# Performance work log

Hardware: AMD Instinct MI355X
Metric: run time of the kernel (lower is better)

The kernel has to match this reference:

```python
import jax, jax.numpy as jnp
import numpy as np

FRAME_LENGTH = 800
FRAME_STEP = 200
FFT_LENGTH = 800


def _hann_window(n):
    # tf.signal.hann_window default: periodic=True -> 0.5 - 0.5*cos(2*pi*k/n)
    k = jnp.arange(n, dtype=jnp.float32)
    return 0.5 - 0.5 * jnp.cos(2.0 * np.pi * k / n)


def setup_inputs() -> dict:
    key = jax.random.key(0)
    signals = jax.random.normal(key, (16, 240000), dtype=jnp.float32)
    window = _hann_window(FRAME_LENGTH)  # fft_length == frame_length, no pad
    n = jnp.arange(FFT_LENGTH, dtype=jnp.float32)
    angles = -2.0 * np.pi * n[:, None] * n[None, :] / float(FFT_LENGTH)  # [k, n]
    dft_cos = jnp.cos(angles)
    dft_sin = jnp.sin(angles)
    return {"signals": signals, "window": window, "dft_cos": dft_cos, "dft_sin": dft_sin}


def reference(signals, window, dft_cos, dft_sin):
    # Frame the signal: [B, num_frames, frame_length] via gather (pad_end=False)
    signal_length = signals.shape[1]
    num_frames = (signal_length - FRAME_LENGTH) // FRAME_STEP + 1
    starts = jnp.arange(num_frames, dtype=jnp.int32) * FRAME_STEP
    offsets = jnp.arange(FRAME_LENGTH, dtype=jnp.int32)
    idx = starts[:, None] + offsets[None, :]          # [F, L]
    frames = signals[:, idx]                          # [B, F, L]
    windowed = frames * window[:FRAME_LENGTH]         # [B, F, L]
    # Dense real/imag DFT: out[b,f,k] = sum_n windowed[b,f,n] * dft[k,n]
    real = jnp.einsum('bfn,kn->bfk', windowed, dft_cos)
    imag = jnp.einsum('bfn,kn->bfk', windowed, dft_sin)
    bins = FFT_LENGTH // 2 + 1
    return jnp.stack([real[:, :, :bins], imag[:, :, :bins]], axis=-1)  # [B, F, bins, 2]
```

## Files before the change

kernel.cpp:

```cpp
#include <hip/hip_runtime.h>
#include <hip/hip_bf16.h>

#define NBATCH   16
#define SIGLEN   240000
#define FRAMES   1197
#define M_TOTAL  (NBATCH * FRAMES)
#define K_TOTAL  800
#define NBINS    401
#define NOUT     (2 * NBINS)
#define FSTEP    200

#define KPAD  832
#define NTK   26
#define GBN   64
#define GNT   13
#define BSTR  840
#define NRG   1197
#define SCSTR 68

#define TMB   512
#define TMT   38
#define TNWG  (GNT * TMT)

#define GMB   1024
#define GMT   19
#define GNWG  (GNT * GMT)

#define SIG_ELEMS  ((size_t)NBATCH * SIGLEN)
#define B_WS_ELEMS ((size_t)(GNT * GBN) * KPAD)
#define APK_ELEMS  ((size_t)NRG * NTK * 64 * 8)
#define WS_TIER1   ((APK_ELEMS + B_WS_ELEMS) * 2)
#define WS_TIER2   ((SIG_ELEMS + B_WS_ELEMS) * 2)

#define PREP_B_BLOCKS 338
#define PREP_SIG_BLOCKS 1875
#define PACK_TOTAL (NRG * NTK * 64)
#define PACK_BLOCKS ((PACK_TOTAL + 255) / 256)

typedef float  f32x4  __attribute__((ext_vector_type(4)));
typedef __bf16 bf16x8 __attribute__((ext_vector_type(8)));

static __device__ __forceinline__ unsigned f2bf_pair(float lo, float hi) {
    union { float f; unsigned u; } a, b;
    a.f = lo; b.f = hi;
    unsigned ua = (a.u + 0x7fffu + ((a.u >> 16) & 1u)) >> 16;
    unsigned ub = (b.u + 0x7fffu + ((b.u >> 16) & 1u)) >> 16;
    return ua | (ub << 16);
}

__global__ __launch_bounds__(256) void prep_b(
    const float* __restrict__ dcos, const float* __restrict__ dsin,
    const float* __restrict__ wnd, ushort* __restrict__ B)
{
    int idx = blockIdx.x * 256 + threadIdx.x;
    int j  = idx / 104;
    int c8 = (idx - j * 104) * 8;
    uint4 p;
    if (j < NOUT && c8 < K_TOTAL) {
        const float* src = ((j & 1) ? dsin : dcos) + (size_t)(j >> 1) * K_TOTAL + c8;
        const float4 s0 = *(const float4*)(src);
        const float4 s1 = *(const float4*)(src + 4);
        const float4 w0 = *(const float4*)(wnd + c8);
        const float4 w1 = *(const float4*)(wnd + c8 + 4);
        p.x = f2bf_pair(s0.x * w0.x, s0.y * w0.y);
        p.y = f2bf_pair(s0.z * w0.z, s0.w * w0.w);
        p.z = f2bf_pair(s1.x * w1.x, s1.y * w1.y);
        p.w = f2bf_pair(s1.z * w1.z, s1.w * w1.w);
    } else {
        p = make_uint4(0u, 0u, 0u, 0u);
    }
    *(uint4*)(B + (size_t)j * KPAD + c8) = p;
}

__global__ __launch_bounds__(256) void prep_pack(
    const float* __restrict__ sig, ushort* __restrict__ Apk)
{
    int idx = blockIdx.x * 256 + threadIdx.x;
    if (idx >= PACK_TOTAL) return;
    const int lane   = idx & 63;
    const int kk     = (idx >> 6) % NTK;
    const int rowgrp = idx / (64 * NTK);
    const int row = rowgrp * 16 + (lane & 15);
    const int bb  = row / FRAMES, ff = row - bb * FRAMES;
    size_t off = (size_t)bb * SIGLEN + ff * FSTEP + kk * 32 + (lane >> 4) * 8;
    if (off > SIG_ELEMS - 8) off = SIG_ELEMS - 8;
    const float4 s0 = *(const float4*)(sig + off);
    const float4 s1 = *(const float4*)(sig + off + 4);
    uint4 p;
    p.x = f2bf_pair(s0.x, s0.y);
    p.y = f2bf_pair(s0.z, s0.w);
    p.z = f2bf_pair(s1.x, s1.y);
    p.w = f2bf_pair(s1.z, s1.w);
    *(uint4*)(Apk + (size_t)idx * 8) = p;
}

__global__ __launch_bounds__(512, 2) void stft_gemm_pk6(
    const ushort* __restrict__ Apk, const ushort* __restrict__ Bw,
    float* __restrict__ out)
{
    __shared__ ushort Bs[GBN * BSTR];

    const int tid  = threadIdx.x;

    const int orig = blockIdx.x;
    const int xcd  = orig & 7;
    const int idx  = orig >> 3;
    const int lbid = (xcd < 6 ? xcd * 62 : 372 + (xcd - 6) * 61) + idx;

    const int ntile = lbid % GNT;
    const int mblk  = lbid / GNT;
    const int j0    = ntile * GBN;
    const int m0    = mblk * TMB;

    const int wave = tid >> 6;
    const int lane = tid & 63;
    const int lr   = lane & 15;
    const int lg   = lane >> 4;
    const int mrow = m0 + wave * 64;

    const int g0 = (m0 >> 4) + wave * 4;
    unsigned aBase[4];
    #pragma unroll
    for (int i = 0; i < 4; ++i) {
        int g = g0 + i;
        if (g >= NRG) g = NRG - 1;
        aBase[i] = (unsigned)g * (NTK * 512) + lane * 8;
    }

    f32x4 acc[4][4];
    #pragma unroll
    for (int i = 0; i < 4; ++i)
        #pragma unroll
        for (int jj = 0; jj < 4; ++jj)
            acc[i][jj] = (f32x4){0.f, 0.f, 0.f, 0.f};

#define LOADA(A_, step) do {                                        \
        _Pragma("unroll")                                           \
        for (int i = 0; i < 4; ++i)                                 \
            A_[i] = *(const bf16x8*)(Apk + (size_t)aBase[i] + (step) * 512); \
    } while (0)

#define LOADB(B_, step) do {                                        \
        const int kofs_ = (step) * 32;                              \
        _Pragma("unroll")                                           \
        for (int jj = 0; jj < 4; ++jj)                              \
            B_[jj] = *(const bf16x8*)&Bs[jj * (16 * BSTR) + lr * BSTR + lg * 8 + kofs_]; \
    } while (0)

#define MM(A_, B_) do {                                             \
        __builtin_amdgcn_s_setprio(1);                              \
        _Pragma("unroll")                                           \
        for (int i = 0; i < 4; ++i)                                 \
            _Pragma("unroll")                                       \
            for (int jj = 0; jj < 4; ++jj)                          \
                acc[i][jj] = __builtin_amdgcn_mfma_f32_16x16x32_bf16( \
                    A_[i], B_[jj], acc[i][jj], 0, 0, 0);            \
        __builtin_amdgcn_s_setprio(0);                              \
    } while (0)

    bf16x8 aX[4], aY[4], bX[4], bY[4];

    LOADA(aX, 0);
    LOADA(aY, 1);

    #pragma unroll
    for (int it = 0; it < 13; ++it) {
        int c   = tid + 512 * it;
        int row = c / 104;
        int col = (c - row * 104) * 8;
        *(uint4*)&Bs[row * BSTR + col] =
            *(const uint4*)(Bw + (size_t)(j0 + row) * KPAD + col);
    }
    __syncthreads();

    LOADB(bX, 0);
    LOADB(bY, 1);

    #pragma unroll 1
    for (int t = 0; t < NTK - 2; t += 2) {
        MM(aX, bX);
        LOADA(aX, t + 2);
        LOADB(bX, t + 2);
        MM(aY, bY);
        LOADA(aY, t + 3);
        LOADB(bY, t + 3);
    }
    MM(aX, bX);
    MM(aY, bY);

#undef LOADA
#undef LOADB
#undef MM

    __syncthreads();
    float* sc = (float*)Bs + wave * (16 * SCSTR);
    const int rl = lane >> 2;
    const int kq = lane & 3;

    #pragma unroll
    for (int i = 0; i < 4; ++i) {
        __builtin_amdgcn_sched_barrier(0);
        #pragma unroll
        for (int jj = 0; jj < 4; ++jj)
            #pragma unroll
            for (int r = 0; r < 4; ++r)
                sc[(lg * 4 + r) * SCSTR + jj * 16 + lr] = acc[i][jj][r];
        asm volatile("s_waitcnt lgkmcnt(0)" ::: "memory");
        __builtin_amdgcn_sched_barrier(0);
        int row = mrow + i * 16 + rl;
        if (row < M_TOTAL) {
            float* op = out + (size_t)row * NOUT;
            #pragma unroll
            for (int ch = 0; ch < 4; ++ch) {
                int colb = j0 + ch * 16 + kq * 4;
                float4 v = *(float4*)&sc[rl * SCSTR + ch * 16 + kq * 4];
                if (colb + 3 < NOUT) {
                    *(float4*)(op + colb) = v;
                } else {
                    #pragma unroll
                    for (int e = 0; e < 4; ++e)
                        if (colb + e < NOUT) op[colb + e] = ((float*)&v)[e];
                }
            }
        }
        asm volatile("s_waitcnt lgkmcnt(0)" ::: "memory");
        __builtin_amdgcn_sched_barrier(0);
    }
}

__global__ __launch_bounds__(256) void prep_all(
    const float* __restrict__ sig, const float* __restrict__ wnd,
    const float* __restrict__ dcos, const float* __restrict__ dsin,
    ushort* __restrict__ sbf, ushort* __restrict__ B)
{
    const int blk = blockIdx.x;
    if (blk < PREP_SIG_BLOCKS) {
        size_t i8 = ((size_t)blk * 256 + threadIdx.x) * 8;
        const float4 s0 = *(const float4*)(sig + i8);
        const float4 s1 = *(const float4*)(sig + i8 + 4);
        uint4 p;
        p.x = f2bf_pair(s0.x, s0.y);
        p.y = f2bf_pair(s0.z, s0.w);
        p.z = f2bf_pair(s1.x, s1.y);
        p.w = f2bf_pair(s1.z, s1.w);
        *(uint4*)(sbf + i8) = p;
    } else {
        int idx = (blk - PREP_SIG_BLOCKS) * 256 + threadIdx.x;
        int j  = idx / 104;
        int c8 = (idx - j * 104) * 8;
        uint4 p;
        if (j < NOUT && c8 < K_TOTAL) {
            const float* src = ((j & 1) ? dsin : dcos) + (size_t)(j >> 1) * K_TOTAL + c8;
            const float4 s0 = *(const float4*)(src);
            const float4 s1 = *(const float4*)(src + 4);
            const float4 w0 = *(const float4*)(wnd + c8);
            const float4 w1 = *(const float4*)(wnd + c8 + 4);
            p.x = f2bf_pair(s0.x * w0.x, s0.y * w0.y);
            p.y = f2bf_pair(s0.z * w0.z, s0.w * w0.w);
            p.z = f2bf_pair(s1.x * w1.x, s1.y * w1.y);
            p.w = f2bf_pair(s1.z * w1.z, s1.w * w1.w);
        } else {
            p = make_uint4(0u, 0u, 0u, 0u);
        }
        *(uint4*)(B + (size_t)j * KPAD + c8) = p;
    }
}

__global__ __launch_bounds__(1024, 4) void stft_gemm_bp5(
    const ushort* __restrict__ sigbf, const ushort* __restrict__ Bw,
    float* __restrict__ out)
{
    __shared__ ushort Bs[GBN * BSTR];

    const int tid  = threadIdx.x;
    const int orig = blockIdx.x;
    const int xcd  = orig & 7;
    const int idx  = orig >> 3;
    const int lbid = (xcd < 7 ? xcd * 31 : 217 + (xcd - 7) * 30) + idx;

    const int ntile = lbid % GNT;
    const int mblk  = lbid / GNT;
    const int j0    = ntile * GBN;
    const int m0    = mblk * GMB;

    const int wave = tid >> 6;
    const int lane = tid & 63;
    const int lr   = lane & 15;
    const int lg   = lane >> 4;
    const int mrow = m0 + wave * 64;

    unsigned aOfs[4];
    #pragma unroll
    for (int i = 0; i < 4; ++i) {
        int row = mrow + i * 16 + lr;
        if (row >= M_TOTAL) row = M_TOTAL - 1;
        int bb = row / FRAMES, ff = row - bb * FRAMES;
        aOfs[i] = (unsigned)(bb * SIGLEN + ff * FSTEP + lg * 8);
    }
    const int bBase = lr * BSTR + lg * 8;

    f32x4 acc[4][4];
    #pragma unroll
    for (int i = 0; i < 4; ++i)
        #pragma unroll
        for (int jj = 0; jj < 4; ++jj)
            acc[i][jj] = (f32x4){0.f, 0.f, 0.f, 0.f};

#define LOADA(A_, step) do {                                        \
        const int kofs_ = (step) * 32;                              \
        _Pragma("unroll")                                           \
        for (int i = 0; i < 4; ++i)                                 \
            A_[i] = *(const bf16x8*)(sigbf + aOfs[i] + kofs_);      \
    } while (0)

#define LOADB(B_, step) do {                                        \
        const int kofs_ = (step) * 32;                              \
        _Pragma("unroll")                                           \
        for (int jj = 0; jj < 4; ++jj)                              \
            B_[jj] = *(const bf16x8*)&Bs[jj * (16 * BSTR) + bBase + kofs_]; \
    } while (0)

#define MM(A_, B_) do {                                             \
        __builtin_amdgcn_s_setprio(1);                              \
        _Pragma("unroll")                                           \
        for (int i = 0; i < 4; ++i)                                 \
            _Pragma("unroll")                                       \
            for (int jj = 0; jj < 4; ++jj)                          \
                acc[i][jj] = __builtin_amdgcn_mfma_f32_16x16x32_bf16( \
                    A_[i], B_[jj], acc[i][jj], 0, 0, 0);            \
        __builtin_amdgcn_s_setprio(0);                              \
    } while (0)

    bf16x8 aX[4], aY[4], bX[4];

    LOADA(aX, 0);
    LOADA(aY, 1);

    #pragma unroll
    for (int it = 0; it < 6; ++it) {
        int c   = tid + 1024 * it;
        int row = c / 104;
        int col = (c - row * 104) * 8;
        *(uint4*)&Bs[row * BSTR + col] =
            *(const uint4*)(Bw + (size_t)(j0 + row) * KPAD + col);
    }
    if (tid < 512) {
        int c   = tid + 6144;
        int row = c / 104;
        int col = (c - row * 104) * 8;
        *(uint4*)&Bs[row * BSTR + col] =
            *(const uint4*)(Bw + (size_t)(j0 + row) * KPAD + col);
    }
    __syncthreads();

    #pragma unroll 1
    for (int t = 0; t < NTK - 2; t += 2) {
        LOADB(bX, t);
        MM(aX, bX);
        LOADA(aX, t + 2);
        LOADB(bX, t + 1);
        MM(aY, bX);
        LOADA(aY, t + 3);
    }
    LOADB(bX, 24); MM(aX, bX);
    LOADB(bX, 25); MM(aY, bX);

#undef LOADA
#undef LOADB
#undef MM

    #pragma unroll
    for (int i = 0; i < 4; ++i) {
        #pragma unroll
        for (int jj = 0; jj < 4; ++jj) {
            int col = j0 + jj * 16 + lr;
            if (col >= NOUT) continue;
            #pragma unroll
            for (int r = 0; r < 4; ++r) {
                int row = mrow + i * 16 + lg * 4 + r;
                if (row < M_TOTAL)
                    out[(size_t)row * NOUT + col] = acc[i][jj][r];
            }
        }
    }
}

#define BM 128
#define BN 128
#define BK 32
#define NTILES_N 7
#define NTILES_M 150
#define NWG (NTILES_M * NTILES_N)
#define LDSS 40
__global__ __launch_bounds__(256) void stft_gemm_fb(
    const float* __restrict__ sig, const float* __restrict__ wnd,
    const float* __restrict__ dcos, const float* __restrict__ dsin,
    float* __restrict__ out)
{
    __shared__ ushort As[BM * LDSS];
    __shared__ ushort Bs[BN * LDSS];
    __shared__ int rowBase[BM];

    const int tid = threadIdx.x;
    const int bid = blockIdx.x;
    const int mt  = bid / NTILES_N;
    const int nt  = bid - mt * NTILES_N;
    const int m0  = mt * BM;
    const int j0  = nt * BN;

    if (tid < BM) {
        int m = m0 + tid;
        int v = -1;
        if (m < M_TOTAL) {
            int b  = m / FRAMES;
            int fl = m - b * FRAMES;
            v = b * SIGLEN + fl * FSTEP;
        }
        rowBase[tid] = v;
    }

    const int rS = tid >> 1;
    const int hS = tid & 1;

    const float* bRow = nullptr;
    {
        int j = j0 + rS;
        if (j < NOUT) {
            const float* srcm = (j & 1) ? dsin : dcos;
            bRow = srcm + (size_t)(j >> 1) * K_TOTAL;
        }
    }

    const int lane = tid & 63;
    const int wave = tid >> 6;
    const int wm   = wave >> 1;
    const int wn   = wave & 1;
    const int lr   = lane & 15;
    const int lg   = lane >> 4;

    f32x4 acc[4][4];
    #pragma unroll
    for (int i = 0; i < 4; ++i)
        #pragma unroll
        for (int jj = 0; jj < 4; ++jj)
            acc[i][jj] = (f32x4){0.f, 0.f, 0.f, 0.f};

    __syncthreads();

    for (int k0 = 0; k0 < K_TOTAL; k0 += BK) {
        {
            int base = rowBase[rS];
            float4 f0, f1, f2, f3;
            if (base >= 0) {
                const float4* sp = (const float4*)(sig + base + k0 + hS * 16);
                f0 = sp[0]; f1 = sp[1]; f2 = sp[2]; f3 = sp[3];
            } else {
                f0 = make_float4(0.f,0.f,0.f,0.f); f1 = f0; f2 = f0; f3 = f0;
            }
            const float4* wp = (const float4*)(wnd + k0 + hS * 16);
            float4 w0 = wp[0], w1 = wp[1], w2 = wp[2], w3 = wp[3];
            uint4 p0, p1;
            p0.x = f2bf_pair(f0.x * w0.x, f0.y * w0.y);
            p0.y = f2bf_pair(f0.z * w0.z, f0.w * w0.w);
            p0.z = f2bf_pair(f1.x * w1.x, f1.y * w1.y);
            p0.w = f2bf_pair(f1.z * w1.z, f1.w * w1.w);
            p1.x = f2bf_pair(f2.x * w2.x, f2.y * w2.y);
            p1.y = f2bf_pair(f2.z * w2.z, f2.w * w2.w);
            p1.z = f2bf_pair(f3.x * w3.x, f3.y * w3.y);
            p1.w = f2bf_pair(f3.z * w3.z, f3.w * w3.w);
            uint4* dst = (uint4*)&As[rS * LDSS + hS * 16];
            dst[0] = p0; dst[1] = p1;
        }
        {
            uint4 p0, p1;
            if (bRow) {
                const float4* sp = (const float4*)(bRow + k0 + hS * 16);
                float4 f0 = sp[0], f1 = sp[1], f2 = sp[2], f3 = sp[3];
                p0.x = f2bf_pair(f0.x, f0.y);
                p0.y = f2bf_pair(f0.z, f0.w);
                p0.z = f2bf_pair(f1.x, f1.y);
                p0.w = f2bf_pair(f1.z, f1.w);
                p1.x = f2bf_pair(f2.x, f2.y);
                p1.y = f2bf_pair(f2.z, f2.w);
                p1.z = f2bf_pair(f3.x, f3.y);
                p1.w = f2bf_pair(f3.z, f3.w);
            } else {
                p0 = make_uint4(0u,0u,0u,0u); p1 = p0;
            }
            uint4* dst = (uint4*)&Bs[rS * LDSS + hS * 16];
            dst[0] = p0; dst[1] = p1;
        }
        __syncthreads();

        bf16x8 a[4], b[4];
        #pragma unroll
        for (int i = 0; i < 4; ++i)
            a[i] = *(const bf16x8*)&As[(wm * 64 + i * 16 + lr) * LDSS + lg * 8];
        #pragma unroll
        for (int i = 0; i < 4; ++i)
            b[i] = *(const bf16x8*)&Bs[(wn * 64 + i * 16 + lr) * LDSS + lg * 8];
        #pragma unroll
        for (int i = 0; i < 4; ++i)
            #pragma unroll
            for (int jj = 0; jj < 4; ++jj)
                acc[i][jj] = __builtin_amdgcn_mfma_f32_16x16x32_bf16(a[i], b[jj], acc[i][jj], 0, 0, 0);

        __syncthreads();
    }

    const int mb = m0 + wm * 64;
    const int jb = j0 + wn * 64;
    #pragma unroll
    for (int i = 0; i < 4; ++i) {
        #pragma unroll
        for (int jj = 0; jj < 4; ++jj) {
            int col = jb + jj * 16 + lr;
            if (col >= NOUT) continue;
            #pragma unroll
            for (int r = 0; r < 4; ++r) {
                int row = mb + i * 16 + lg * 4 + r;
                if (row < M_TOTAL)
                    out[(size_t)row * NOUT + col] = acc[i][jj][r];
            }
        }
    }
}

extern "C" void kernel_launch(void* const* d_in, const int* in_sizes, int n_in,
                              void* d_out, int out_size, void* d_ws, size_t ws_size,
                              hipStream_t stream) {
    const float* sig  = (const float*)d_in[0];
    const float* wnd  = (const float*)d_in[1];
    const float* dcos = (const float*)d_in[2];
    const float* dsin = (const float*)d_in[3];
    float* out = (float*)d_out;

    if (ws_size >= WS_TIER1 && d_ws != nullptr) {
        ushort* Apk = (ushort*)d_ws;
        ushort* Bws = Apk + APK_ELEMS;
        prep_b<<<dim3(PREP_B_BLOCKS), dim3(256), 0, stream>>>(dcos, dsin, wnd, Bws);
        prep_pack<<<dim3(PACK_BLOCKS), dim3(256), 0, stream>>>(sig, Apk);
        stft_gemm_pk6<<<dim3(TNWG), dim3(512), 0, stream>>>(Apk, Bws, out);
    } else if (ws_size >= WS_TIER2 && d_ws != nullptr) {
        ushort* sbf = (ushort*)d_ws;
        ushort* Bws = sbf + SIG_ELEMS;
        prep_all<<<dim3(PREP_SIG_BLOCKS + PREP_B_BLOCKS), dim3(256), 0, stream>>>(
            sig, wnd, dcos, dsin, sbf, Bws);
        stft_gemm_bp5<<<dim3(GNWG), dim3(1024), 0, stream>>>(sbf, Bws, out);
    } else {
        stft_gemm_fb<<<dim3(NWG), dim3(256), 0, stream>>>(sig, wnd, dcos, dsin, out);
    }
}
```

Before: 66.22 us.

## Widen GEMM N-tile to 128 with two-phase K-half B staging in LDS

The main GEMM's output tile grows from 64 to 128 columns, so each workgroup computes 4x8 MFMA tiles per wave and each A fragment loaded from global memory is reused twice as often. The grid shrinks from 13x38 to 7x38 workgroups. To fit LDS, the B tile is staged in two K halves with extra barriers between phases, and B fragments are no longer double-buffered in registers. Accumulator registers double, which risks occupancy and spills, and the N padding to 896 adds some wasted columns and a longer B prep.

```diff
diff --git a/kernel.cpp b/kernel.cpp
--- a/kernel.cpp
+++ b/kernel.cpp
@@ -12,27 +12,33 @@
 
 #define KPAD  832
 #define NTK   26
+#define NRG   1197
+
+#define TBN   128
+#define TNT   7
+#define NPAD2 (TNT * TBN)
+#define TMB   512
+#define TMT   38
+#define TNWG  (TNT * TMT)
+#define KHALF 416
+#define BHSTR 424
+#define SC2   132
+
 #define GBN   64
 #define GNT   13
-#define BSTR  840
-#define NRG   1197
-#define SCSTR 68
-
-#define TMB   512
-#define TMT   38
-#define TNWG  (GNT * TMT)
-
 #define GMB   1024
 #define GMT   19
 #define GNWG  (GNT * GMT)
+#define BSTR  840
 
 #define SIG_ELEMS  ((size_t)NBATCH * SIGLEN)
-#define B_WS_ELEMS ((size_t)(GNT * GBN) * KPAD)
+#define B_WS_ELEMS ((size_t)NPAD2 * KPAD)
+#define B2_WS_ELEMS ((size_t)(GNT * GBN) * KPAD)
 #define APK_ELEMS  ((size_t)NRG * NTK * 64 * 8)
 #define WS_TIER1   ((APK_ELEMS + B_WS_ELEMS) * 2)
-#define WS_TIER2   ((SIG_ELEMS + B_WS_ELEMS) * 2)
-
-#define PREP_B_BLOCKS 338
+#define WS_TIER2   ((SIG_ELEMS + B2_WS_ELEMS) * 2)
+
+#define PREP_B_BLOCKS  (NPAD2 * 104 / 256)
 #define PREP_SIG_BLOCKS 1875
 #define PACK_TOTAL (NRG * NTK * 64)
 #define PACK_BLOCKS ((PACK_TOTAL + 255) / 256)
@@ -94,22 +100,22 @@
     *(uint4*)(Apk + (size_t)idx * 8) = p;
 }
 
-__global__ __launch_bounds__(512, 2) void stft_gemm_pk6(
+__global__ __launch_bounds__(512, 2) void stft_gemm_w128(
     const ushort* __restrict__ Apk, const ushort* __restrict__ Bw,
     float* __restrict__ out)
 {
-    __shared__ ushort Bs[GBN * BSTR];
+    __shared__ ushort Bs[TBN * BHSTR];
 
     const int tid  = threadIdx.x;
 
     const int orig = blockIdx.x;
     const int xcd  = orig & 7;
     const int idx  = orig >> 3;
-    const int lbid = (xcd < 6 ? xcd * 62 : 372 + (xcd - 6) * 61) + idx;
-
-    const int ntile = lbid % GNT;
-    const int mblk  = lbid / GNT;
-    const int j0    = ntile * GBN;
+    const int lbid = (xcd < 2 ? xcd * 34 : 68 + (xcd - 2) * 33) + idx;
+
+    const int ntile = lbid % TNT;
+    const int mblk  = lbid / TNT;
+    const int j0    = ntile * TBN;
     const int m0    = mblk * TMB;
 
     const int wave = tid >> 6;
@@ -126,25 +132,26 @@
         if (g >= NRG) g = NRG - 1;
         aBase[i] = (unsigned)g * (NTK * 512) + lane * 8;
     }
-
-    f32x4 acc[4][4];
+    const int bBase = lr * BHSTR + lg * 8;
+
+    f32x4 acc[4][8];
     #pragma unroll
     for (int i = 0; i < 4; ++i)
         #pragma unroll
-        for (int jj = 0; jj < 4; ++jj)
+        for (int jj = 0; jj < 8; ++jj)
             acc[i][jj] = (f32x4){0.f, 0.f, 0.f, 0.f};
 
 #define LOADA(A_, step) do {                                        \
+        const int s_ = (step) <= 25 ? (step) : 25;                  \
         _Pragma("unroll")                                           \
         for (int i = 0; i < 4; ++i)                                 \
-            A_[i] = *(const bf16x8*)(Apk + (size_t)aBase[i] + (step) * 512); \
-    } while (0)
-
-#define LOADB(B_, step) do {                                        \
-        const int kofs_ = (step) * 32;                              \
-        _Pragma("unroll")                                           \
-        for (int jj = 0; jj < 4; ++jj)                              \
-            B_[jj] = *(const bf16x8*)&Bs[jj * (16 * BSTR) + lr * BSTR + lg * 8 + kofs_]; \
+            A_[i] = *(const bf16x8*)(Apk + (size_t)aBase[i] + s_ * 512); \
+    } while (0)
+
+#define LOADB(B_, sl) do {                                          \
+        _Pragma("unroll")                                           \
+        for (int jj = 0; jj < 8; ++jj)                              \
+            B_[jj] = *(const bf16x8*)&Bs[jj * (16 * BHSTR) + bBase + (sl) * 32]; \
     } while (0)
 
 #define MM(A_, B_) do {                                             \
@@ -152,48 +159,67 @@
         _Pragma("unroll")                                           \
         for (int i = 0; i < 4; ++i)                                 \
             _Pragma("unroll")                                       \
-            for (int jj = 0; jj < 4; ++jj)                          \
+            for (int jj = 0; jj < 8; ++jj)                          \
                 acc[i][jj] = __builtin_amdgcn_mfma_f32_16x16x32_bf16( \
                     A_[i], B_[jj], acc[i][jj], 0, 0, 0);            \
         __builtin_amdgcn_s_setprio(0);                              \
     } while (0)
 
-    bf16x8 aX[4], aY[4], bX[4], bY[4];
+#define STAGEB(kh) do {                                             \
+        _Pragma("unroll")                                           \
+        for (int it = 0; it < 13; ++it) {                           \
+            int c   = tid + 512 * it;                    \
+            int row = c / 52;                                        \
+            int col = (c - row * 52) * 8;                            \
+            *(uint4*)&Bs[row * BHSTR + col] =                        \
+                *(const uint4*)(Bw + (size_t)(j0 + row) * KPAD + (kh) * KHALF + col); \
+        }                                                            \
+    } while (0)
+
+    bf16x8 aX[4], aY[4], bX[8];
 
     LOADA(aX, 0);
     LOADA(aY, 1);
 
-    #pragma unroll
-    for (int it = 0; it < 13; ++it) {
-        int c   = tid + 512 * it;
-        int row = c / 104;
-        int col = (c - row * 104) * 8;
-        *(uint4*)&Bs[row * BSTR + col] =
-            *(const uint4*)(Bw + (size_t)(j0 + row) * KPAD + col);
-    }
+    STAGEB(0);
     __syncthreads();
 
-    LOADB(bX, 0);
-    LOADB(bY, 1);
-
     #pragma unroll 1
-    for (int t = 0; t < NTK - 2; t += 2) {
+    for (int t = 0; t < 12; t += 2) {
+        LOADB(bX, t);
         MM(aX, bX);
         LOADA(aX, t + 2);
-        LOADB(bX, t + 2);
-        MM(aY, bY);
+        LOADB(bX, t + 1);
+        MM(aY, bX);
         LOADA(aY, t + 3);
-        LOADB(bY, t + 3);
-    }
+    }
+    LOADB(bX, 12);
     MM(aX, bX);
-    MM(aY, bY);
+    LOADA(aX, 14);
+
+    __syncthreads();
+    STAGEB(1);
+    __syncthreads();
+
+    #pragma unroll 1
+    for (int t = 13; t < 25; t += 2) {
+        LOADB(bX, t - 13);
+        MM(aY, bX);
+        LOADA(aY, t + 2);
+        LOADB(bX, t - 12);
+        MM(aX, bX);
+        LOADA(aX, t + 3);
+    }
+    LOADB(bX, 12);
+    MM(aY, bX);
 
 #undef LOADA
 #undef LOADB
 #undef MM
+#undef STAGEB
 
     __syncthreads();
-    float* sc = (float*)Bs + wave * (16 * SCSTR);
+    float* sc = (float*)Bs + wave * (16 * SC2);
     const int rl = lane >> 2;
     const int kq = lane & 3;
 
@@ -201,19 +227,19 @@
     for (int i = 0; i < 4; ++i) {
         __builtin_amdgcn_sched_barrier(0);
         #pragma unroll
-        for (int jj = 0; jj < 4; ++jj)
+        for (int jj = 0; jj < 8; ++jj)
             #pragma unroll
             for (int r = 0; r < 4; ++r)
-                sc[(lg * 4 + r) * SCSTR + jj * 16 + lr] = acc[i][jj][r];
+                sc[(lg * 4 + r) * SC2 + jj * 16 + lr] = acc[i][jj][r];
         asm volatile("s_waitcnt lgkmcnt(0)" ::: "memory");
         __builtin_amdgcn_sched_barrier(0);
         int row = mrow + i * 16 + rl;
         if (row < M_TOTAL) {
             float* op = out + (size_t)row * NOUT;
             #pragma unroll
-            for (int ch = 0; ch < 4; ++ch) {
+            for (int ch = 0; ch < 8; ++ch) {
                 int colb = j0 + ch * 16 + kq * 4;
-                float4 v = *(float4*)&sc[rl * SCSTR + ch * 16 + kq * 4];
+                float4 v = *(float4*)&sc[rl * SC2 + ch * 16 + kq * 4];
                 if (colb + 3 < NOUT) {
                     *(float4*)(op + colb) = v;
                 } else {
@@ -540,7 +566,7 @@
         ushort* Bws = Apk + APK_ELEMS;
         prep_b<<<dim3(PREP_B_BLOCKS), dim3(256), 0, stream>>>(dcos, dsin, wnd, Bws);
         prep_pack<<<dim3(PACK_BLOCKS), dim3(256), 0, stream>>>(sig, Apk);
-        stft_gemm_pk6<<<dim3(TNWG), dim3(512), 0, stream>>>(Apk, Bws, out);
+        stft_gemm_w128<<<dim3(TNWG), dim3(512), 0, stream>>>(Apk, Bws, out);
     } else if (ws_size >= WS_TIER2 && d_ws != nullptr) {
         ushort* sbf = (ushort*)d_ws;
         ushort* Bws = sbf + SIG_ELEMS;
```

New measurement: 97.06 us. +46.6%, slower.
